# Optimization experiments

Measured on AMD Instinct MI355X. Metric: run time of the kernel, lower is better.

The kernel has to match this reference:

```python
import jax, jax.numpy as jnp
import numpy as np

EPS = 1e-5


def _mamba(x, in_w, conv_w, conv_b, x_w, dt_w, dt_b, A_log, D, out_w):
    # x: [B, L, d_model] -> [B, L, d_model]; mamba_ssm defaults (bias-free in/out proj)
    Bsz, L, _ = x.shape
    d_inner, d_conv = conv_w.shape
    dt_rank = dt_w.shape[1]
    N = A_log.shape[1]

    xz = x @ in_w.T                              # [B, L, 2*d_inner]
    u, z = jnp.split(xz, 2, axis=-1)

    # causal depthwise conv (torch pads both sides by d_conv-1 then slices [:L])
    uc = jnp.pad(u.transpose(0, 2, 1), ((0, 0), (0, 0), (d_conv - 1, 0)))  # [B, d, L+pad]
    uc = jax.lax.conv_general_dilated(
        uc, conv_w[:, None, :], window_strides=(1,), padding='VALID',
        feature_group_count=d_inner, dimension_numbers=('NCH', 'OIH', 'NCH'))
    u = jax.nn.silu(uc + conv_b[None, :, None]).transpose(0, 2, 1)          # [B, L, d]

    xdbc = u @ x_w.T                              # [B, L, dt_rank + 2N]
    dt, Bm, Cm = jnp.split(xdbc, [dt_rank, dt_rank + N], axis=-1)
    delta = jax.nn.softplus(dt @ dt_w.T + dt_b)   # [B, L, d]

    A = -jnp.exp(A_log)                           # [d, N]
    dA = jnp.exp(delta[..., None] * A)            # [B, L, d, N]
    dBu = delta[..., None] * Bm[:, :, None, :] * u[..., None]  # [B, L, d, N]

    def step(h, inp):
        dA_t, dBu_t, C_t = inp
        h = dA_t * h + dBu_t                      # [B, d, N]
        y = jnp.einsum('bdn,bn->bd', h, C_t)
        return h, y

    h0 = jnp.zeros((Bsz, d_inner, N), dA.dtype)
    _, ys = jax.lax.scan(step, h0,
                         (dA.transpose(1, 0, 2, 3), dBu.transpose(1, 0, 2, 3), Cm.transpose(1, 0, 2)))
    y = ys.transpose(1, 0, 2)                     # [B, L, d]
    y = (y + u * D) * jax.nn.silu(z)
    return y @ out_w.T


def reference(x, input_lengths, m, emb, conv_w, conv_b, ln_g, ln_b,
              f_in_w, f_conv_w, f_conv_b, f_x_w, f_dt_w, f_dt_b, f_A_log, f_D, f_out_w,
              b_in_w, b_conv_w, b_conv_b, b_x_w, b_dt_w, b_dt_b, b_A_log, b_D, b_out_w,
              proj_w, proj_b):
    K = conv_w.shape[-1]
    pad = (K - 1) // 2
    h = emb[x].transpose(0, 2, 1)                 # [B, C, L]
    for i in range(conv_w.shape[0]):
        h = jax.lax.conv_general_dilated(h, conv_w[i], (1,), [(pad, pad)],
                                         dimension_numbers=('NCH', 'OIH', 'NCH'))
        h = h + conv_b[i][None, :, None]
        mu = h.mean(axis=1, keepdims=True)
        var = ((h - mu) ** 2).mean(axis=1, keepdims=True)
        h = (h - mu) * jax.lax.rsqrt(var + EPS)
        h = h * ln_g[i][None, :, None] + ln_b[i][None, :, None]
        h = jnp.where(h > 0, h, 0.2 * h)          # LeakyReLU(0.2); dropout is eval no-op
        h = jnp.where(m[:, None, :], 0.0, h)
    h = h.transpose(0, 2, 1)                      # [B, L, C]
    fo = _mamba(h, f_in_w, f_conv_w, f_conv_b, f_x_w, f_dt_w, f_dt_b, f_A_log, f_D, f_out_w)
    bo = _mamba(h[:, ::-1], b_in_w, b_conv_w, b_conv_b, b_x_w, b_dt_w, b_dt_b, b_A_log, b_D, b_out_w)
    comb = jnp.concatenate([fo, bo], axis=-1) @ proj_w.T + proj_b
    return jnp.where(m[:, :, None], 0.0, comb)


def setup_inputs() -> dict:
    key = jax.random.key(0)
    ks = iter(jax.random.split(key, 40))
    B, L, C, K, depth, V = 4, 1024, 512, 5, 3, 178
    d_inner, d_state, d_conv, dt_rank = 2 * C, 16, 4, 32
    inp = {
        'x': jax.random.randint(next(ks), (B, L), 0, V),
        'input_lengths': jax.random.randint(next(ks), (B,), 1, L + 1),
        'm': jnp.zeros((B, L), dtype=bool),
        'emb': jax.random.normal(next(ks), (V, C)),
        'conv_w': jax.random.normal(next(ks), (depth, C, C, K)) * 0.05,
        'conv_b': jax.random.normal(next(ks), (depth, C)) * 0.05,
        'ln_g': jnp.ones((depth, C)),
        'ln_b': jnp.zeros((depth, C)),
        'proj_w': jax.random.normal(next(ks), (C, 2 * C)) * 0.02,
        'proj_b': jax.random.normal(next(ks), (C,)) * 0.02,
    }
    for p in ('f', 'b'):
        inp[p + '_in_w'] = jax.random.normal(next(ks), (2 * d_inner, C)) * 0.02
        inp[p + '_conv_w'] = jax.random.normal(next(ks), (d_inner, d_conv)) * 0.1
        inp[p + '_conv_b'] = jax.random.normal(next(ks), (d_inner,)) * 0.1
        inp[p + '_x_w'] = jax.random.normal(next(ks), (dt_rank + 2 * d_state, d_inner)) * 0.02
        inp[p + '_dt_w'] = jax.random.normal(next(ks), (d_inner, dt_rank)) * 0.02
        inp[p + '_dt_b'] = jax.random.normal(next(ks), (d_inner,)) * 0.1
        inp[p + '_A_log'] = jax.random.uniform(next(ks), (d_inner, d_state))
        inp[p + '_D'] = jax.random.normal(next(ks), (d_inner,)) * 0.1
        inp[p + '_out_w'] = jax.random.normal(next(ks), (C, d_inner)) * 0.02
    return inp
```

## Files before the change

### kernel.cpp

```cpp
#include <hip/hip_runtime.h>
#include <hip/hip_bf16.h>

typedef __attribute__((ext_vector_type(8))) short short8;
typedef __attribute__((ext_vector_type(4))) float f32x4;
typedef __attribute__((ext_vector_type(4))) unsigned short ushort4_t;

#define BSZ 4
#define LSEQ 1024
#define CCH 512
#define BL (BSZ*LSEQ)
#define BL2 (2*BL)
#define DI 1024
#define NST 16
#define DTR 32
#define NCH 32
#define CLEN 32

__device__ __forceinline__ float sigmoidf_(float x){ return 1.f/(1.f+__expf(-x)); }
__device__ __forceinline__ float softplus_(float x){ return x > 20.f ? x : __logf(1.f + __expf(x)); }
__device__ __forceinline__ float fexp2_(float x){ return __builtin_amdgcn_exp2f(x); }
__device__ __forceinline__ unsigned short f2bf_(float f){
  __hip_bfloat16 h = __float2bfloat16(f); return *(unsigned short*)&h;
}
__device__ __forceinline__ float b2f_(unsigned short s){
  unsigned u = ((unsigned)s) << 16; float f; __builtin_memcpy(&f, &u, 4); return f;
}

typedef const __attribute__((address_space(1))) unsigned int* gas_t;
typedef __attribute__((address_space(3))) unsigned int* las_t;
__device__ __forceinline__ void gload16(const void* g, void* l){
  __builtin_amdgcn_global_load_lds((gas_t)g, (las_t)l, 16, 0, 0);
}


struct CastEnt { const float* s; unsigned short* d; unsigned n4, acc; };
struct CastArgs { CastEnt e[9]; unsigned total4; };
__global__ void k_cast_all(CastArgs a){
  unsigned i = blockIdx.x*256 + threadIdx.x;
  if (i >= a.total4) return;
  #pragma unroll
  for (int k=0;k<9;k++){
    if (i < a.e[k].acc + a.e[k].n4){
      unsigned j = i - a.e[k].acc;
      float4 v = ((const float4*)a.e[k].s)[j];
      ushort4_t o = { f2bf_(v.x), f2bf_(v.y), f2bf_(v.z), f2bf_(v.w) };
      *(ushort4_t*)(a.e[k].d + (size_t)j*4) = o;
      return;
    }
  }
}

__global__ void k_prep_convw(const float* __restrict__ cw, __hip_bfloat16* __restrict__ wt){
  int i = blockIdx.x*256 + threadIdx.x;
  const int total = 3*CCH*CCH*5;
  if (i >= total) return;
  int j = i % (CCH*5);
  int co = (i/(CCH*5)) % CCH;
  int layer = i/(CCH*5*CCH);
  int k = j >> 9, ci = j & 511;
  wt[i] = __float2bfloat16(cw[(((size_t)layer*CCH + co)*CCH + ci)*5 + k]);
}

__global__ void k_embed(const int* __restrict__ x, const float* __restrict__ emb,
                        __hip_bfloat16* __restrict__ xpad0, __hip_bfloat16* __restrict__ xpad1){
  int i = blockIdx.x*256 + threadIdx.x;
  const int total = BSZ*(LSEQ+4)*CCH;
  const int total2 = total + BSZ*4*CCH;
  if (i >= total2) return;
  if (i >= total){
    int j = i - total;
    int c = j & (CCH-1);
    int pr = (j >> 9) & 3;
    int b = j >> 11;
    int rr = (pr < 2) ? pr : (LSEQ+2) + (pr-2);
    xpad1[((size_t)b*(LSEQ+4) + rr)*CCH + c] = __float2bfloat16(0.f);
    return;
  }
  int c = i & (CCH-1);
  int r = (i >> 9) % (LSEQ+4);
  int b = i / ((LSEQ+4)*CCH);
  float v = 0.f;
  if (r >= 2 && r < LSEQ+2){
    int tok = x[b*LSEQ + (r-2)];
    v = emb[(size_t)tok*CCH + c];
  }
  xpad0[i] = __float2bfloat16(v);
}

__global__ __launch_bounds__(256) void k_ln(
    const float* __restrict__ in, const float* __restrict__ in2,
    const float* __restrict__ g, const float* __restrict__ bb,
    const unsigned char* __restrict__ mask,
    __hip_bfloat16* __restrict__ xpad_next,
    __hip_bfloat16* __restrict__ h_enc){
  int row = blockIdx.x;
  int b = row >> 10, l = row & 1023;
  const float* xr = in + (size_t)row*CCH;
  const float* xr2 = in2 + (size_t)row*CCH;
  int t = threadIdx.x;
  float v0 = xr[t] + xr2[t], v1 = xr[t+256] + xr2[t+256];
  float s = v0+v1, s2 = v0*v0 + v1*v1;
  #pragma unroll
  for (int off=32; off>0; off>>=1){ s += __shfl_down(s,off); s2 += __shfl_down(s2,off); }
  __shared__ float ls[8];
  if ((t&63)==0){ ls[t>>6] = s; ls[(t>>6)+4] = s2; }
  __syncthreads();
  float S  = ls[0]+ls[1]+ls[2]+ls[3];
  float S2 = ls[4]+ls[5]+ls[6]+ls[7];
  float mu = S*(1.f/CCH);
  float var = S2*(1.f/CCH) - mu*mu;
  float rs = rsqrtf(var + 1e-5f);
  bool mk = mask[row] != 0;
  #pragma unroll
  for (int e=0; e<2; e++){
    int c = t + e*256;
    float v = e ? v1 : v0;
    float h = (v-mu)*rs*g[c] + bb[c];
    h = h > 0.f ? h : 0.2f*h;
    if (mk) h = 0.f;
    __hip_bfloat16 hb = __float2bfloat16(h);
    if (xpad_next) xpad_next[((size_t)b*(LSEQ+4) + (l+2))*CCH + c] = hb;
    if (h_enc) h_enc[(size_t)row*CCH + c] = hb;
  }
}

__global__ __launch_bounds__(256) void k_gemm_ksplit(
    const __hip_bfloat16* __restrict__ A, int lda,
    const __hip_bfloat16* __restrict__ W, size_t wStride,
    float* __restrict__ Cout, int ldc, int K, unsigned short* __restrict__ dtb){
  __shared__ float red[4*1024];
  int m0 = blockIdx.x << 4;
  const __hip_bfloat16* Wd = W + (size_t)(m0 >> 12)*wStride;
  int tid = threadIdx.x;
  int w = tid >> 6, lane = tid & 63;
  int r = lane & 15, kg = lane >> 4;
  int Kw = K >> 2;
  int kbase = w*Kw;

  const short* Ap = (const short*)A + (size_t)(m0 + r)*lda + kbase + kg*8;
  const short* Wp[4];
  #pragma unroll
  for (int nj=0; nj<4; nj++)
    Wp[nj] = (const short*)Wd + (size_t)(nj*16 + r)*K + kbase + kg*8;

  f32x4 acc[4];
  #pragma unroll
  for (int nj=0;nj<4;nj++) acc[nj] = (f32x4){0.f,0.f,0.f,0.f};

  for (int kk=0; kk<Kw; kk+=32){
    short8 a = *(const short8*)(Ap + kk);
    #pragma unroll
    for (int nj=0;nj<4;nj++){
      short8 wv = *(const short8*)(Wp[nj] + kk);
      acc[nj] = __builtin_amdgcn_mfma_f32_16x16x32_bf16(a, wv, acc[nj], 0,0,0);
    }
  }
  #pragma unroll
  for (int nj=0;nj<4;nj++)
    #pragma unroll
    for (int reg=0; reg<4; reg++){
      int rowt = kg*4 + reg;
      int col  = nj*16 + r;
      red[w*1024 + rowt*64 + col] = acc[nj][reg];
    }
  __syncthreads();
  int e0 = tid*4;
  f32x4 s = *(const f32x4*)&red[e0];
  #pragma unroll
  for (int ww=1; ww<4; ww++){
    f32x4 p = *(const f32x4*)&red[ww*1024 + e0];
    s.x += p.x; s.y += p.y; s.z += p.z; s.w += p.w;
  }
  int rowt = e0 >> 6, col = e0 & 63;
  *(f32x4*)&Cout[(size_t)(m0+rowt)*ldc + col] = s;
  if (col < 32){
    ushort4_t o = { f2bf_(s.x), f2bf_(s.y), f2bf_(s.z), f2bf_(s.w) };
    *(ushort4_t*)&dtb[(size_t)(m0+rowt)*32 + col] = o;
  }
}

template<bool OUTBF>
__global__ __launch_bounds__(256) void k_gemm_big(
    const __hip_bfloat16* __restrict__ A, int lda, int padExtra, int revA,
    const __hip_bfloat16* __restrict__ W, size_t wStride,
    void* __restrict__ C0, void* __restrict__ C1, size_t segBytes, int ldc, int coloff,
    int tiles_n, int baseBlocks, int totalBlocks, int Kc, int Kb,
    const float* __restrict__ bias0, const float* __restrict__ bias1, int act,
    const unsigned char* __restrict__ mask, int outRowSub, int dirColOff, int uzMode){
  __shared__ alignas(16) __hip_bfloat16 smem[3][6144];
  int b = blockIdx.x;
  int wg = (b & 7)*(totalBlocks >> 3) + (b >> 3);
  int seg = wg / baseBlocks;
  int bid = wg - seg*baseBlocks;
  int tn = bid % tiles_n;
  int tm = bid / tiles_n;
  int m0 = tm*128, n0 = tn*64;
  int dir = m0 >> 12;
  int kOff = seg*Kc;
  const __hip_bfloat16* Wd = W + (size_t)dir*wStride;
  void* Cout = (void*)((char*)C0 + (size_t)seg*segBytes);
  const float* bsel = dir ? bias1 : bias0;
  const float* biasp = (bsel && seg==0) ? bsel : nullptr;

  int tid = threadIdx.x;
  int wid = tid >> 6, lane = tid & 63;
  int r = lane & 15, kg = lane >> 4;

  int sr = lane >> 2;
  int gs = (lane & 3) ^ ((sr >> 1) & 3);
  auto physrow = [&](int ar)->int{
    if (revA && ar >= 4096){
      int r2 = ar - 4096;
      return (r2 & ~1023) | (1023 - (r2 & 1023));
    }
    return ar + padExtra*(ar >> 10);
  };
  int arow0 = m0 + wid*16 + sr;
  int arow1 = arow0 + 64;
  size_t aoff0 = (size_t)physrow(arow0)*lda + kOff + gs*8;
  size_t aoff1 = (size_t)physrow(arow1)*lda + kOff + gs*8;
  int bcol = n0 + wid*16 + sr;
  size_t boff = (size_t)bcol*Kb + kOff + gs*8;

  int wr = wid >> 1, wc = wid & 1;
  int xs = (kg ^ ((r >> 1) & 3))*8;
  int afrag[4], bfrag[2];
  #pragma unroll
  for (int mi=0; mi<4; mi++) afrag[mi] = (wr*64 + mi*16 + r)*32 + xs;
  #pragma unroll
  for (int nj=0; nj<2; nj++) bfrag[nj] = 4096 + (wc*32 + nj*16 + r)*32 + xs;

  f32x4 acc[4][2];
  #pragma unroll
  for (int mi=0;mi<4;mi++)
    #pragma unroll
    for (int nj=0;nj<2;nj++) acc[mi][nj] = (f32x4){0.f,0.f,0.f,0.f};

  const int nt = Kc >> 5;
  auto stage = [&](int kt, int bufi){
    __hip_bfloat16* sb = &smem[bufi][0];
    int k0 = kt*32;
    gload16((const short*)A + aoff0 + k0, sb + wid*512);
    gload16((const short*)A + aoff1 + k0, sb + (wid+4)*512);
    gload16((const short*)W + (size_t)(Wd - W) + boff + k0, sb + 4096 + wid*512);
  };
  auto compute = [&](int bufi){
    const __hip_bfloat16* sb = &smem[bufi][0];
    short8 a[4], bb2[2];
    #pragma unroll
    for (int mi=0;mi<4;mi++) a[mi] = *(const short8*)&sb[afrag[mi]];
    #pragma unroll
    for (int nj=0;nj<2;nj++) bb2[nj] = *(const short8*)&sb[bfrag[nj]];
    #pragma unroll
    for (int mi=0;mi<4;mi++)
      #pragma unroll
      for (int nj=0;nj<2;nj++)
        acc[mi][nj] = __builtin_amdgcn_mfma_f32_16x16x32_bf16(a[mi], bb2[nj], acc[mi][nj], 0,0,0);
  };

  if (nt >= 3){
    stage(0, 0);
    stage(1, 1);
    int bi = 0;
    #pragma unroll 1
    for (int t=0; t<nt; t++){
      if (t+1 < nt) asm volatile("s_waitcnt vmcnt(3)" ::: "memory");
      else          asm volatile("s_waitcnt vmcnt(0)" ::: "memory");
      __builtin_amdgcn_s_barrier();
      __builtin_amdgcn_sched_barrier(0);
      if (t+2 < nt){
        int nb2 = bi + 2; if (nb2 >= 3) nb2 -= 3;
        stage(t+2, nb2);
      }
      compute(bi);
      bi = (bi+1 == 3) ? 0 : bi+1;
    }
  } else {
    for (int s=0; s<nt; s++) stage(s, s);
    asm volatile("s_waitcnt vmcnt(0)" ::: "memory");
    __builtin_amdgcn_s_barrier();
    __builtin_amdgcn_sched_barrier(0);
    for (int t=0; t<nt; t++) compute(t);
  }

  #pragma unroll
  for (int mi=0;mi<4;mi++){
    #pragma unroll
    for (int nj=0;nj<2;nj++){
      #pragma unroll
      for (int reg=0; reg<4; reg++){
        int row = m0 + wr*64 + mi*16 + kg*4 + reg;
        int col = n0 + wc*32 + nj*16 + r;
        float v = acc[mi][nj][reg];
        if (uzMode){
          if (col < 1024) ((__hip_bfloat16*)C0)[(size_t)row*1024 + col] = __float2bfloat16(v);
          else            ((__hip_bfloat16*)C1)[(size_t)row*1024 + (col-1024)] = __float2bfloat16(v);
          continue;
        }
        if (biasp) v += biasp[col];
        if (act == 1) v = softplus_(v);
        int row_out = row - dir*outRowSub;
        if (mask && mask[row_out]) v = 0.f;
        size_t o = (size_t)row_out*ldc + coloff + dir*dirColOff + col;
        if (OUTBF) ((__hip_bfloat16*)Cout)[o] = __float2bfloat16(v);
        else       ((float*)Cout)[o] = v;
      }
    }
  }
}


__global__ void k_dwconv(const unsigned short* __restrict__ upre,
                         const float* __restrict__ cw0, const float* __restrict__ cw1,
                         const float* __restrict__ cb0, const float* __restrict__ cb1,
                         __hip_bfloat16* __restrict__ ub){
  int i = blockIdx.x*256 + threadIdx.x;
  if (i >= BL2*DI/4) return;
  int d4 = i & (DI/4 - 1);
  int d = d4 << 2;
  int row = i >> 8;
  int dir = row >> 12;
  const float* cw = (dir ? cw1 : cw0) + d*4;
  const float* cb = (dir ? cb1 : cb0) + d;
  int l = row & 1023;
  int rb = row & ~1023;
  f32x4 cwv[4];
  #pragma unroll
  for (int j=0;j<4;j++) cwv[j] = *(const f32x4*)&cw[j*4];
  f32x4 acc = *(const f32x4*)cb;
  #pragma unroll
  for (int k=0;k<4;k++){
    int ll = l - 3 + k;
    if (ll >= 0){
      ushort4_t xv = *(const ushort4_t*)&upre[(size_t)(rb + ll)*DI + d];
      acc.x = __fmaf_rn(cwv[0][k], b2f_(xv.x), acc.x);
      acc.y = __fmaf_rn(cwv[1][k], b2f_(xv.y), acc.y);
      acc.z = __fmaf_rn(cwv[2][k], b2f_(xv.z), acc.z);
      acc.w = __fmaf_rn(cwv[3][k], b2f_(xv.w), acc.w);
    }
  }
  f32x4 s;
  s.x = acc.x * sigmoidf_(acc.x);
  s.y = acc.y * sigmoidf_(acc.y);
  s.z = acc.z * sigmoidf_(acc.z);
  s.w = acc.w * sigmoidf_(acc.w);
  ushort4_t o = { f2bf_(s.x), f2bf_(s.y), f2bf_(s.z), f2bf_(s.w) };
  *(ushort4_t*)((unsigned short*)ub + (size_t)i*4) = o;
}


__global__ __launch_bounds__(256) void k_scan_part(
    const float* __restrict__ Alog0, const float* __restrict__ Alog1,
    const unsigned short* __restrict__ dyb, const unsigned short* __restrict__ ub,
    const float* __restrict__ xdbc,
    float* __restrict__ Hp, float* __restrict__ Pp){
  __shared__ alignas(16) float Bsh[CLEN*16];
  int t = threadIdx.x;
  int dblk = blockIdx.x & 3;
  int c = (blockIdx.x >> 2) & (NCH-1);
  int b8 = blockIdx.x >> 7;
  const float* A_log = (b8 >> 2) ? Alog1 : Alog0;
  int d = dblk*256 + t;
  size_t blbase = (size_t)b8*LSEQ + (size_t)c*CLEN;
  if (t < CLEN*4){
    int l = t >> 2, q = t & 3;
    *(f32x4*)&Bsh[l*16 + q*4] = *(const f32x4*)&xdbc[(blbase+l)*64 + 32 + q*4];
  }
  float Af[16];
  #pragma unroll
  for (int n=0; n<16; n+=4){
    f32x4 a = *(const f32x4*)&A_log[(size_t)d*16 + n];
    Af[n]   = -__expf(a.x)*1.442695041f; Af[n+1] = -__expf(a.y)*1.442695041f;
    Af[n+2] = -__expf(a.z)*1.442695041f; Af[n+3] = -__expf(a.w)*1.442695041f;
  }
  float h[16];
  #pragma unroll
  for (int n=0;n<16;n++) h[n]=0.f;
  float Sdv = 0.f;
  const unsigned short* dyp = dyb + blbase*DI + d;
  const unsigned short* ubp = ub + blbase*DI + d;
  float dvb[2][8], uvb[2][8];
  #pragma unroll
  for (int j=0;j<8;j++){ dvb[0][j] = b2f_(dyp[(size_t)j*DI]); uvb[0][j] = b2f_(ubp[(size_t)j*DI]); }
  __syncthreads();
  #pragma unroll
  for (int g=0; g<4; g++){
    int cur = g & 1;
    if (g+1 < 4){
      int nxt = cur ^ 1;
      #pragma unroll
      for (int j=0;j<8;j++){
        size_t l = (size_t)(g+1)*8 + j;
        dvb[nxt][j] = b2f_(dyp[l*DI]); uvb[nxt][j] = b2f_(ubp[l*DI]);
      }
    }
    #pragma unroll
    for (int j=0;j<8;j++){
      int l = g*8 + j;
      float dv = dvb[cur][j], uv = uvb[cur][j];
      float duv = dv*uv;
      Sdv += dv;
      #pragma unroll
      for (int n=0;n<16;n++){
        float dA = fexp2_(dv*Af[n]);
        h[n] = __fmaf_rn(dA, h[n], duv*Bsh[l*16+n]);
      }
    }
  }
  size_t pb = (((size_t)(b8*NCH + c))*DI + d)*16;
  #pragma unroll
  for (int n=0;n<16;n+=4){
    *(f32x4*)&Hp[pb+n] = (f32x4){h[n],h[n+1],h[n+2],h[n+3]};
    *(f32x4*)&Pp[pb+n] = (f32x4){fexp2_(Af[n]*Sdv), fexp2_(Af[n+1]*Sdv),
                                 fexp2_(Af[n+2]*Sdv), fexp2_(Af[n+3]*Sdv)};
  }
}

__global__ void k_scan_comb(float* __restrict__ Hp, float* __restrict__ Pp){
  int i = blockIdx.x*256 + threadIdx.x;
  if (i >= BL2*NST) return;
  int n = i & 15, row = i >> 4;
  int b8 = row >> 10, d = row & 1023;
  float hin = 0.f;
  #pragma unroll
  for (int c=0;c<NCH;c++){
    size_t idx = (((size_t)(b8*NCH + c))*DI + d)*16 + n;
    float P = Pp[idx], H = Hp[idx];
    Pp[idx] = hin;
    hin = __fmaf_rn(P, hin, H);
  }
}

__global__ __launch_bounds__(256) void k_scan_fin(
    const float* __restrict__ Alog0, const float* __restrict__ Alog1,
    const unsigned short* __restrict__ dyb, const unsigned short* __restrict__ ub,
    const float* __restrict__ xdbc,
    const float* __restrict__ Hin, const unsigned short* __restrict__ zb,
    const float* __restrict__ Dp0, const float* __restrict__ Dp1,
    __hip_bfloat16* __restrict__ yb){
  __shared__ alignas(16) float BCsh[CLEN*32];
  int t = threadIdx.x;
  int dblk = blockIdx.x & 3;
  int c = (blockIdx.x >> 2) & (NCH-1);
  int b8 = blockIdx.x >> 7;
  int dirb = b8 >> 2;
  const float* A_log = dirb ? Alog1 : Alog0;
  const float* Dp = dirb ? Dp1 : Dp0;
  int d = dblk*256 + t;
  size_t blbase = (size_t)b8*LSEQ + (size_t)c*CLEN;
  {
    int l = t >> 3, q = t & 7;
    *(f32x4*)&BCsh[l*32 + q*4] = *(const f32x4*)&xdbc[(blbase+l)*64 + 32 + q*4];
  }
  float Af[16];
  #pragma unroll
  for (int n=0; n<16; n+=4){
    f32x4 a = *(const f32x4*)&A_log[(size_t)d*16 + n];
    Af[n]   = -__expf(a.x)*1.442695041f; Af[n+1] = -__expf(a.y)*1.442695041f;
    Af[n+2] = -__expf(a.z)*1.442695041f; Af[n+3] = -__expf(a.w)*1.442695041f;
  }
  size_t pb = (((size_t)(b8*NCH + c))*DI + d)*16;
  float h[16];
  #pragma unroll
  for (int n=0;n<16;n+=4){
    f32x4 hv = *(const f32x4*)&Hin[pb+n];
    h[n]=hv.x; h[n+1]=hv.y; h[n+2]=hv.z; h[n+3]=hv.w;
  }
  float Dd = Dp[d];
  const unsigned short* dyp = dyb + blbase*DI + d;
  const unsigned short* ubp = ub + blbase*DI + d;
  const unsigned short* zp  = zb + blbase*DI + d;
  float dvb[2][8], uvb[2][8], zvb[2][8];
  #pragma unroll
  for (int j=0;j<8;j++){
    dvb[0][j] = b2f_(dyp[(size_t)j*DI]);
    uvb[0][j] = b2f_(ubp[(size_t)j*DI]);
    zvb[0][j] = b2f_(zp[(size_t)j*DI]);
  }
  __syncthreads();
  #pragma unroll
  for (int g=0; g<4; g++){
    int cur = g & 1;
    if (g+1 < 4){
      int nxt = cur ^ 1;
      #pragma unroll
      for (int j=0;j<8;j++){
        size_t l = (size_t)(g+1)*8 + j;
        dvb[nxt][j] = b2f_(dyp[l*DI]);
        uvb[nxt][j] = b2f_(ubp[l*DI]);
        zvb[nxt][j] = b2f_(zp[l*DI]);
      }
    }
    #pragma unroll
    for (int j=0;j<8;j++){
      int l = g*8 + j;
      float dv = dvb[cur][j], uv = uvb[cur][j], zv = zvb[cur][j];
      float duv = dv*uv;
      float y = 0.f;
      #pragma unroll
      for (int n=0;n<16;n++){
        float dA = fexp2_(dv*Af[n]);
        h[n] = __fmaf_rn(dA, h[n], duv*BCsh[l*32+n]);
        y = __fmaf_rn(h[n], BCsh[l*32+16+n], y);
      }
      float gg = zv * sigmoidf_(zv);
      float out = __fmaf_rn(uv, Dd, y) * gg;
      yb[(blbase+l)*DI + d] = __float2bfloat16(out);
    }
  }
}


extern "C" void kernel_launch(void* const* d_in, const int* in_sizes, int n_in,
                              void* d_out, int out_size, void* d_ws, size_t ws_size,
                              hipStream_t stream){
  (void)in_sizes; (void)n_in; (void)out_size; (void)ws_size;
  const int*   x     = (const int*)d_in[0];
  const unsigned char* m = (const unsigned char*)d_in[2];
  const float* emb   = (const float*)d_in[3];
  const float* convw = (const float*)d_in[4];
  const float* convb = (const float*)d_in[5];
  const float* lng   = (const float*)d_in[6];
  const float* lnb   = (const float*)d_in[7];
  const float* projw = (const float*)d_in[8];
  const float* projb = (const float*)d_in[9];

  char* ws = (char*)d_ws;
  size_t off = 0;
  auto alloc = [&](size_t bytes)->char*{
    char* p = ws + off; off += (bytes + 255) & ~((size_t)255); return p;
  };
  auto wt_conv = (__hip_bfloat16*)alloc((size_t)3*CCH*CCH*5*2);
  auto w_in2  = (__hip_bfloat16*)alloc((size_t)2*2*DI*CCH*2);
  auto w_x2   = (__hip_bfloat16*)alloc((size_t)2*64*DI*2);
  auto w_dt2  = (__hip_bfloat16*)alloc((size_t)2*DI*DTR*2);
  auto w_out2 = (__hip_bfloat16*)alloc((size_t)2*CCH*DI*2);
  auto w_proj = (__hip_bfloat16*)alloc((size_t)CCH*1024*2);
  auto xpad0  = (__hip_bfloat16*)alloc((size_t)BSZ*(LSEQ+4)*CCH*2);
  auto xpad1  = (__hip_bfloat16*)alloc((size_t)BSZ*(LSEQ+4)*CCH*2);
  auto scr    = (float*)alloc((size_t)8*NCH*DI*NST*4);
  auto h_enc  = (__hip_bfloat16*)alloc((size_t)BL*CCH*2);
  auto upre   = (unsigned short*)alloc((size_t)BL2*DI*2);
  auto zb     = (unsigned short*)alloc((size_t)BL2*DI*2);
  auto ub2    = (__hip_bfloat16*)alloc((size_t)BL2*DI*2);
  auto xdbc2  = (float*)alloc((size_t)BL2*64*4);
  auto dtb2   = (unsigned short*)alloc((size_t)BL2*DTR*2);
  auto dy2    = (unsigned short*)alloc((size_t)BL2*DI*2);
  auto convp1 = (float*)alloc((size_t)BL*CCH*4);
  auto yb2    = (__hip_bfloat16*)alloc((size_t)BL2*DI*2);
  auto fob    = (__hip_bfloat16*)alloc((size_t)BL*DI*2);
  auto Pp     = (float*)alloc((size_t)8*NCH*DI*NST*4);

  float* Hp = scr;

  auto nb = [](size_t n){ return (unsigned)((n + 255)/256); };

  k_prep_convw<<<dim3(nb((size_t)3*CCH*CCH*5)), dim3(256), 0, stream>>>(convw, wt_conv);
  {
    CastArgs ca;
    unsigned acc = 0;
    auto put = [&](int k, const void* s, void* d, unsigned n4){
      ca.e[k].s = (const float*)s; ca.e[k].d = (unsigned short*)d;
      ca.e[k].n4 = n4; ca.e[k].acc = acc; acc += n4;
    };
    for (int dir=0; dir<2; dir++){
      int base = 10 + 9*dir;
      put(dir*4+0, d_in[base+0], (unsigned short*)w_in2  + (size_t)dir*2*DI*CCH, (2*DI*CCH)/4);
      put(dir*4+1, d_in[base+3], (unsigned short*)w_x2   + (size_t)dir*64*DI,    (64*DI)/4);
      put(dir*4+2, d_in[base+4], (unsigned short*)w_dt2  + (size_t)dir*DI*DTR,   (DI*DTR)/4);
      put(dir*4+3, d_in[base+8], (unsigned short*)w_out2 + (size_t)dir*CCH*DI,   (CCH*DI)/4);
    }
    put(8, projw, w_proj, (CCH*1024)/4);
    ca.total4 = acc;
    k_cast_all<<<dim3(nb(acc)), dim3(256), 0, stream>>>(ca);
  }

  auto gemm_big = [&](const void* A, int lda, int padE, int revA, const void* W, size_t wStride,
                  void* C0, void* C1, size_t segBytes, int ldc, int coloff,
                  int M, int N, int Kc, int Kb, int nSeg,
                  const float* bias0, const float* bias1, int act,
                  const unsigned char* msk, int outRowSub, int dirColOff, bool outbf, int uzMode){
    int tiles_n = N/64;
    int baseBlocks = (M/128)*tiles_n;
    int blocks = baseBlocks * nSeg;
    if (outbf)
      k_gemm_big<true><<<dim3(blocks), dim3(256), 0, stream>>>((const __hip_bfloat16*)A, lda, padE, revA,
          (const __hip_bfloat16*)W, wStride, C0, C1, segBytes, ldc, coloff, tiles_n, baseBlocks, blocks,
          Kc, Kb, bias0, bias1, act, msk, outRowSub, dirColOff, uzMode);
    else
      k_gemm_big<false><<<dim3(blocks), dim3(256), 0, stream>>>((const __hip_bfloat16*)A, lda, padE, revA,
          (const __hip_bfloat16*)W, wStride, C0, C1, segBytes, ldc, coloff, tiles_n, baseBlocks, blocks,
          Kc, Kb, bias0, bias1, act, msk, outRowSub, dirColOff, uzMode);
  };

  k_embed<<<dim3(nb((size_t)BSZ*(LSEQ+4)*CCH + BSZ*4*CCH)), dim3(256), 0, stream>>>(x, emb, xpad0, xpad1);

  __hip_bfloat16* xp_in = xpad0;
  __hip_bfloat16* xp_out = xpad1;
  const size_t segB_conv = (size_t)((char*)convp1 - (char*)scr);
  for (int layer=0; layer<3; layer++){
    const __hip_bfloat16* wt = wt_conv + (size_t)layer*CCH*CCH*5;
    gemm_big(xp_in, CCH, 4, 0, wt, 0, scr, nullptr, segB_conv, CCH, 0, BL, CCH, 1280, 2560, 2,
             convb + layer*CCH, convb + layer*CCH, 0, nullptr, 0, 0, false, 0);
    bool last = (layer==2);
    k_ln<<<dim3(BL), dim3(256), 0, stream>>>(scr, convp1, lng + layer*CCH, lnb + layer*CCH, m,
        last ? nullptr : xp_out, last ? h_enc : nullptr);
    __hip_bfloat16* t2 = xp_in; xp_in = xp_out; xp_out = t2;
  }

  const float* Alog0 = (const float*)d_in[16];
  const float* Alog1 = (const float*)d_in[25];
  const float* Dp0   = (const float*)d_in[17];
  const float* Dp1   = (const float*)d_in[26];

  gemm_big(h_enc, CCH, 0, 1, w_in2, (size_t)2*DI*CCH, upre, zb, 0, 2*DI, 0,
           BL2, 2*DI, CCH, CCH, 1, nullptr, nullptr, 0, nullptr, 0, 0, false, 1);
  k_dwconv<<<dim3(nb((size_t)BL2*DI/4)), dim3(256), 0, stream>>>(upre,
      (const float*)d_in[11], (const float*)d_in[20],
      (const float*)d_in[12], (const float*)d_in[21], ub2);
  k_gemm_ksplit<<<dim3(BL2/16), dim3(256), 0, stream>>>(ub2, DI, w_x2, (size_t)64*DI, xdbc2, 64, DI, dtb2);
  gemm_big(dtb2, DTR, 0, 0, w_dt2, (size_t)DI*DTR, dy2, nullptr, 0, DI, 0,
           BL2, DI, DTR, DTR, 1, (const float*)d_in[15], (const float*)d_in[24], 1,
           nullptr, 0, 0, true, 0);
  k_scan_part<<<dim3(1024), dim3(256), 0, stream>>>(Alog0, Alog1, dy2, (const unsigned short*)ub2, xdbc2, Hp, Pp);
  k_scan_comb<<<dim3(nb((size_t)BL2*NST)), dim3(256), 0, stream>>>(Hp, Pp);
  k_scan_fin<<<dim3(1024), dim3(256), 0, stream>>>(Alog0, Alog1, dy2, (const unsigned short*)ub2, xdbc2, Pp, zb, Dp0, Dp1, yb2);
  gemm_big(yb2, DI, 0, 0, w_out2, (size_t)CCH*DI, fob, nullptr, 0, DI, 0,
           BL2, CCH, DI, DI, 1, nullptr, nullptr, 0, nullptr, BL, 512, true, 0);

  gemm_big(fob, DI, 0, 0, w_proj, 0, d_out, nullptr, 0, CCH, 0,
           BL, CCH, DI, DI, 1, projb, projb, 0, m, 0, 0, false, 0);
}
```

Measured before the change: 310.3 us.

## Use two-wave 64x64 GEMM tiles and bf16 conv partial outputs

Reorganizes the big GEMM kernel so each of two waves computes a 64x64 sub-tile instead of four waves at 64x32, raising MFMA work per LDS fragment load, and launches it with 128 threads. The conv-layer split-K partial results are now written as bf16 instead of fp32, and LayerNorm reads bf16 inputs, halving that intermediate traffic. Risks are lower occupancy or latency hiding with fewer waves per block, and precision loss from rounding partial sums to bf16 before summation.

```diff
diff --git a/kernel.cpp b/kernel.cpp
--- a/kernel.cpp
+++ b/kernel.cpp
@@ -88,17 +88,17 @@
 }
 
 __global__ __launch_bounds__(256) void k_ln(
-    const float* __restrict__ in, const float* __restrict__ in2,
+    const unsigned short* __restrict__ in, const unsigned short* __restrict__ in2,
     const float* __restrict__ g, const float* __restrict__ bb,
     const unsigned char* __restrict__ mask,
     __hip_bfloat16* __restrict__ xpad_next,
     __hip_bfloat16* __restrict__ h_enc){
   int row = blockIdx.x;
   int b = row >> 10, l = row & 1023;
-  const float* xr = in + (size_t)row*CCH;
-  const float* xr2 = in2 + (size_t)row*CCH;
+  size_t ro = (size_t)row*CCH;
   int t = threadIdx.x;
-  float v0 = xr[t] + xr2[t], v1 = xr[t+256] + xr2[t+256];
+  float v0 = b2f_(in[ro+t]) + b2f_(in2[ro+t]);
+  float v1 = b2f_(in[ro+t+256]) + b2f_(in2[ro+t+256]);
   float s = v0+v1, s2 = v0*v0 + v1*v1;
   #pragma unroll
   for (int off=32; off>0; off>>=1){ s += __shfl_down(s,off); s2 += __shfl_down(s2,off); }
@@ -180,7 +180,7 @@
 }
 
 template<bool OUTBF>
-__global__ __launch_bounds__(256) void k_gemm_big(
+__global__ __launch_bounds__(128) void k_gemm_big(
     const __hip_bfloat16* __restrict__ A, int lda, int padExtra, int revA,
     const __hip_bfloat16* __restrict__ W, size_t wStride,
     void* __restrict__ C0, void* __restrict__ C1, size_t segBytes, int ldc, int coloff,
@@ -215,46 +215,54 @@
     }
     return ar + padExtra*(ar >> 10);
   };
-  int arow0 = m0 + wid*16 + sr;
-  int arow1 = arow0 + 64;
-  size_t aoff0 = (size_t)physrow(arow0)*lda + kOff + gs*8;
-  size_t aoff1 = (size_t)physrow(arow1)*lda + kOff + gs*8;
-  int bcol = n0 + wid*16 + sr;
-  size_t boff = (size_t)bcol*Kb + kOff + gs*8;
-
-  int wr = wid >> 1, wc = wid & 1;
+  size_t aoffq[4];
+  #pragma unroll
+  for (int q=0;q<4;q++){
+    int arow = m0 + wid*64 + q*16 + sr;
+    aoffq[q] = (size_t)physrow(arow)*lda + kOff + gs*8;
+  }
+  size_t boffq[2];
+  #pragma unroll
+  for (int q=0;q<2;q++){
+    int bcol = n0 + wid*32 + q*16 + sr;
+    boffq[q] = (size_t)bcol*Kb + kOff + gs*8;
+  }
+
   int xs = (kg ^ ((r >> 1) & 3))*8;
-  int afrag[4], bfrag[2];
-  #pragma unroll
-  for (int mi=0; mi<4; mi++) afrag[mi] = (wr*64 + mi*16 + r)*32 + xs;
-  #pragma unroll
-  for (int nj=0; nj<2; nj++) bfrag[nj] = 4096 + (wc*32 + nj*16 + r)*32 + xs;
-
-  f32x4 acc[4][2];
+  int afrag[4], bfrag[4];
+  #pragma unroll
+  for (int mi=0; mi<4; mi++) afrag[mi] = (wid*64 + mi*16 + r)*32 + xs;
+  #pragma unroll
+  for (int nj=0; nj<4; nj++) bfrag[nj] = 4096 + (nj*16 + r)*32 + xs;
+
+  f32x4 acc[4][4];
   #pragma unroll
   for (int mi=0;mi<4;mi++)
     #pragma unroll
-    for (int nj=0;nj<2;nj++) acc[mi][nj] = (f32x4){0.f,0.f,0.f,0.f};
+    for (int nj=0;nj<4;nj++) acc[mi][nj] = (f32x4){0.f,0.f,0.f,0.f};
 
   const int nt = Kc >> 5;
   auto stage = [&](int kt, int bufi){
     __hip_bfloat16* sb = &smem[bufi][0];
     int k0 = kt*32;
-    gload16((const short*)A + aoff0 + k0, sb + wid*512);
-    gload16((const short*)A + aoff1 + k0, sb + (wid+4)*512);
-    gload16((const short*)W + (size_t)(Wd - W) + boff + k0, sb + 4096 + wid*512);
+    #pragma unroll
+    for (int q=0;q<4;q++)
+      gload16((const short*)A + aoffq[q] + k0, sb + (wid*64 + q*16)*32);
+    #pragma unroll
+    for (int q=0;q<2;q++)
+      gload16((const short*)W + (size_t)(Wd - W) + boffq[q] + k0, sb + 4096 + (wid*32 + q*16)*32);
   };
   auto compute = [&](int bufi){
     const __hip_bfloat16* sb = &smem[bufi][0];
-    short8 a[4], bb2[2];
+    short8 a[4], bb2[4];
     #pragma unroll
     for (int mi=0;mi<4;mi++) a[mi] = *(const short8*)&sb[afrag[mi]];
     #pragma unroll
-    for (int nj=0;nj<2;nj++) bb2[nj] = *(const short8*)&sb[bfrag[nj]];
+    for (int nj=0;nj<4;nj++) bb2[nj] = *(const short8*)&sb[bfrag[nj]];
     #pragma unroll
     for (int mi=0;mi<4;mi++)
       #pragma unroll
-      for (int nj=0;nj<2;nj++)
+      for (int nj=0;nj<4;nj++)
         acc[mi][nj] = __builtin_amdgcn_mfma_f32_16x16x32_bf16(a[mi], bb2[nj], acc[mi][nj], 0,0,0);
   };
 
@@ -264,7 +272,7 @@
     int bi = 0;
     #pragma unroll 1
     for (int t=0; t<nt; t++){
-      if (t+1 < nt) asm volatile("s_waitcnt vmcnt(3)" ::: "memory");
+      if (t+1 < nt) asm volatile("s_waitcnt vmcnt(6)" ::: "memory");
       else          asm volatile("s_waitcnt vmcnt(0)" ::: "memory");
       __builtin_amdgcn_s_barrier();
       __builtin_amdgcn_sched_barrier(0);
@@ -286,11 +294,11 @@
   #pragma unroll
   for (int mi=0;mi<4;mi++){
     #pragma unroll
-    for (int nj=0;nj<2;nj++){
+    for (int nj=0;nj<4;nj++){
       #pragma unroll
       for (int reg=0; reg<4; reg++){
-        int row = m0 + wr*64 + mi*16 + kg*4 + reg;
-        int col = n0 + wc*32 + nj*16 + r;
+        int row = m0 + wid*64 + mi*16 + kg*4 + reg;
+        int col = n0 + nj*16 + r;
         float v = acc[mi][nj][reg];
         if (uzMode){
           if (col < 1024) ((__hip_bfloat16*)C0)[(size_t)row*1024 + col] = __float2bfloat16(v);
@@ -546,7 +554,7 @@
   auto xdbc2  = (float*)alloc((size_t)BL2*64*4);
   auto dtb2   = (unsigned short*)alloc((size_t)BL2*DTR*2);
   auto dy2    = (unsigned short*)alloc((size_t)BL2*DI*2);
-  auto convp1 = (float*)alloc((size_t)BL*CCH*4);
+  auto convp1 = (unsigned short*)alloc((size_t)BL*CCH*2);
   auto yb2    = (__hip_bfloat16*)alloc((size_t)BL2*DI*2);
   auto fob    = (__hip_bfloat16*)alloc((size_t)BL*DI*2);
   auto Pp     = (float*)alloc((size_t)8*NCH*DI*NST*4);
@@ -584,11 +592,11 @@
     int baseBlocks = (M/128)*tiles_n;
     int blocks = baseBlocks * nSeg;
     if (outbf)
-      k_gemm_big<true><<<dim3(blocks), dim3(256), 0, stream>>>((const __hip_bfloat16*)A, lda, padE, revA,
+      k_gemm_big<true><<<dim3(blocks), dim3(128), 0, stream>>>((const __hip_bfloat16*)A, lda, padE, revA,
           (const __hip_bfloat16*)W, wStride, C0, C1, segBytes, ldc, coloff, tiles_n, baseBlocks, blocks,
           Kc, Kb, bias0, bias1, act, msk, outRowSub, dirColOff, uzMode);
     else
-      k_gemm_big<false><<<dim3(blocks), dim3(256), 0, stream>>>((const __hip_bfloat16*)A, lda, padE, revA,
+      k_gemm_big<false><<<dim3(blocks), dim3(128), 0, stream>>>((const __hip_bfloat16*)A, lda, padE, revA,
           (const __hip_bfloat16*)W, wStride, C0, C1, segBytes, ldc, coloff, tiles_n, baseBlocks, blocks,
           Kc, Kb, bias0, bias1, act, msk, outRowSub, dirColOff, uzMode);
   };
@@ -601,9 +609,10 @@
   for (int layer=0; layer<3; layer++){
     const __hip_bfloat16* wt = wt_conv + (size_t)layer*CCH*CCH*5;
     gemm_big(xp_in, CCH, 4, 0, wt, 0, scr, nullptr, segB_conv, CCH, 0, BL, CCH, 1280, 2560, 2,
-             convb + layer*CCH, convb + layer*CCH, 0, nullptr, 0, 0, false, 0);
+             convb + layer*CCH, convb + layer*CCH, 0, nullptr, 0, 0, true, 0);
     bool last = (layer==2);
-    k_ln<<<dim3(BL), dim3(256), 0, stream>>>(scr, convp1, lng + layer*CCH, lnb + layer*CCH, m,
+    k_ln<<<dim3(BL), dim3(256), 0, stream>>>((const unsigned short*)scr, convp1,
+        lng + layer*CCH, lnb + layer*CCH, m,
         last ? nullptr : xp_out, last ? h_enc : nullptr);
     __hip_bfloat16* t2 = xp_in; xp_in = xp_out; xp_out = t2;
   }
```

Measured after the change: 352.7 us. 13.7% more time.
